# Performance work log

Measured on AMD Instinct MI355X. Metric: run time of the kernel, lower is better.

The kernel has to match this reference:

```python
import jax, jax.numpy as jnp
import numpy as np

N_NODES = 50000
N_EDGES = 800000
FEAT_DIM = 64
NUM_RELS = 8


def setup_inputs() -> dict:
    key = jax.random.key(0)
    k1, k2, k3, k4, k5 = jax.random.split(key, 5)
    features = jax.random.normal(k1, (N_NODES, FEAT_DIM), dtype=jnp.float32)
    # xavier_uniform with relu gain ~= sqrt(2)*sqrt(6/(D+D))
    limit = np.sqrt(2.0) * np.sqrt(6.0 / (FEAT_DIM + FEAT_DIM))
    weight_r = jax.random.uniform(k2, (NUM_RELS, FEAT_DIM, FEAT_DIM), dtype=jnp.float32,
                                  minval=-limit, maxval=limit)
    src = jax.random.randint(k3, (N_EDGES,), 0, N_NODES, dtype=jnp.int64 if jax.config.jax_enable_x64 else jnp.int32)
    dst = jax.random.randint(k4, (N_EDGES,), 0, N_NODES, dtype=src.dtype)
    etype = jax.random.randint(k5, (N_EDGES,), 0, NUM_RELS, dtype=src.dtype)
    return {"features": features, "weight_r": weight_r, "src": src, "dst": dst, "etype": etype}


def reference(features, weight_r, src, dst, etype):
    N, D = features.shape
    c = 0.2
    # in-degree of each destination node (DGL 'deg' node data)
    deg = jax.ops.segment_sum(jnp.ones(dst.shape, dtype=features.dtype), dst, num_segments=N)
    # relation-batched matmul: h @ W_r for every relation, then gather per edge.
    # [R, N, D] = 8*50000*64 floats -- cheap vs. materializing [E, D, D] weights.
    hw = jnp.einsum('nd,rdf->rnf', features, weight_r)
    msg = hw[etype, src] / deg[dst][:, None]          # [E, D]
    M = jax.ops.segment_sum(msg, dst, num_segments=N)  # scatter-sum mailbox reduce
    updated = jax.nn.relu(c * features + (1.0 - c) * M)
    # DGL only applies reduce to nodes that received messages; others keep h.
    return jnp.where((deg > 0)[:, None], updated, features)
```

## Files before the change

### kernel.cpp

```cpp
#include <hip/hip_runtime.h>
#include <hip/hip_bf16.h>

#define N_NODES 50000
#define N_EDGES 800000
#define FEAT 64
#define NRELS 8
#define NBUCK 196
#define EPB 2048
#define NBP 391
#define BCAP 5120
#define FB_BLOCKS 782
#define NPB 32
#define FUSE_BLOCKS 1563

typedef __attribute__((ext_vector_type(8))) short bf16x8;
typedef __attribute__((ext_vector_type(4))) float f32x4;

static __host__ __device__ inline size_t align256(size_t x) { return (x + 255) & ~(size_t)255; }

__device__ inline unsigned short f2b(float f) {
    unsigned u = __builtin_bit_cast(unsigned, f);
    unsigned r = (u + 0x7fffu + ((u >> 16) & 1u)) >> 16;
    return (unsigned short)r;
}
__device__ inline float b2f(unsigned short u) {
    unsigned v = ((unsigned)u) << 16;
    return __builtin_bit_cast(float, v);
}

__global__ void bfill_kernel(const int* __restrict__ dst, const int* __restrict__ srcv,
                             const int* __restrict__ et, const float* __restrict__ W,
                             int* __restrict__ bcnt, int* __restrict__ tmp,
                             unsigned short* __restrict__ WtT, int E) {
    __shared__ int hist[256];
    __shared__ int base[256];
    __shared__ int lcur[256];
    const int t = threadIdx.x;
    hist[t] = 0; lcur[t] = 0;
    __syncthreads();

    const int4* dst4 = (const int4*)dst;
    const int4* src4 = (const int4*)srcv;
    const int4* et4  = (const int4*)et;
    const int n4 = E >> 2;
    int bk[8], pk[8];
#pragma unroll
    for (int k = 0; k < 2; k++) {
        int i4 = blockIdx.x * 512 + t + k * 256;
        if (i4 < n4) {
            int4 d = dst4[i4];
            int4 s = src4[i4];
            int4 r = et4[i4];
            const int dd[4] = {d.x, d.y, d.z, d.w};
            const int ss[4] = {s.x, s.y, s.z, s.w};
            const int rr[4] = {r.x, r.y, r.z, r.w};
#pragma unroll
            for (int j = 0; j < 4; j++) {
                int idx = k * 4 + j;
                bk[idx] = dd[j] >> 8;
                pk[idx] = (ss[j] & 0xFFFF) | (rr[j] << 16) | ((dd[j] & 255) << 19);
                atomicAdd(&hist[bk[idx]], 1);
            }
        } else {
#pragma unroll
            for (int j = 0; j < 4; j++) bk[k * 4 + j] = -1;
        }
    }
    __syncthreads();
    if (t < NBUCK && hist[t] > 0)
        base[t] = t * BCAP + atomicAdd(&bcnt[t], hist[t]);
    __syncthreads();
#pragma unroll
    for (int k = 0; k < 8; k++) {
        if (bk[k] >= 0) {
            int r = atomicAdd(&lcur[bk[k]], 1);
            int pos = base[bk[k]] + r;
            if (pos < (bk[k] + 1) * BCAP)
                tmp[pos] = pk[k];
        }
    }

    if (blockIdx.x < 32) {
        int i4 = blockIdx.x * 256 + t;
        float4 v = ((const float4*)W)[i4];
        int bse = i4 * 4;
        int f0 = bse & 63;
        int rd = bse >> 6;
        int d  = rd & 63;
        int r  = rd >> 6;
        unsigned short* w0 = WtT + ((size_t)(r * 64 + f0) * 64 + d);
        w0[0 * 64] = f2b(v.x);
        w0[1 * 64] = f2b(v.y);
        w0[2 * 64] = f2b(v.z);
        w0[3 * 64] = f2b(v.w);
    }
}

__global__ void mid_kernel(const int* __restrict__ bcnt, const int* __restrict__ tmp,
                           int* __restrict__ spk, int* __restrict__ off_s,
                           int* __restrict__ off_e,
                           const float* __restrict__ feat,
                           unsigned short* __restrict__ Fb, int N) {
    __shared__ int hist[2048];
    __shared__ int s[256];
    const int t = threadIdx.x;

    if (blockIdx.x < NBUCK) {
        const int b = blockIdx.x;
        const int n0 = b * 256;
        const int nn = min(256, N - n0);
        const int s0 = b * BCAP;
        const int s1 = s0 + min(bcnt[b], BCAP);

#pragma unroll
        for (int j = 0; j < 8; j++) hist[t * 8 + j] = 0;
        __syncthreads();
        for (int i = s0 + t; i < s1; i += 1024) {
            int v0 = tmp[i];
            int v1 = (i + 256 < s1) ? tmp[i + 256] : -1;
            int v2 = (i + 512 < s1) ? tmp[i + 512] : -1;
            int v3 = (i + 768 < s1) ? tmp[i + 768] : -1;
            atomicAdd(&hist[(v0 >> 16) & 0x7FF], 1);
            if (v1 >= 0) atomicAdd(&hist[(v1 >> 16) & 0x7FF], 1);
            if (v2 >= 0) atomicAdd(&hist[(v2 >> 16) & 0x7FF], 1);
            if (v3 >= 0) atomicAdd(&hist[(v3 >> 16) & 0x7FF], 1);
        }
        __syncthreads();
        int loc[8], st[8], T = 0;
#pragma unroll
        for (int j = 0; j < 8; j++) loc[j] = hist[t * 8 + j];
#pragma unroll
        for (int j = 0; j < 8; j++) { st[j] = T; T += loc[j]; }
        s[t] = T;
        __syncthreads();
        for (int o = 1; o < 256; o <<= 1) {
            int u = (t >= o) ? s[t - o] : 0;
            __syncthreads();
            s[t] += u;
            __syncthreads();
        }
        const int base = s0 + s[t] - T;
        if (t < nn) {
            off_s[n0 + t] = base;
            off_e[n0 + t] = base + T;
        }
#pragma unroll
        for (int j = 0; j < 8; j++) hist[t * 8 + j] = base + st[j];
        __syncthreads();
        for (int i = s0 + t; i < s1; i += 1024) {
            int v0 = tmp[i];
            int v1 = (i + 256 < s1) ? tmp[i + 256] : -1;
            int v2 = (i + 512 < s1) ? tmp[i + 512] : -1;
            int v3 = (i + 768 < s1) ? tmp[i + 768] : -1;
            int p0 = atomicAdd(&hist[(v0 >> 16) & 0x7FF], 1);
            spk[p0] = v0;
            if (v1 >= 0) { int p1 = atomicAdd(&hist[(v1 >> 16) & 0x7FF], 1); spk[p1] = v1; }
            if (v2 >= 0) { int p2 = atomicAdd(&hist[(v2 >> 16) & 0x7FF], 1); spk[p2] = v2; }
            if (v3 >= 0) { int p3 = atomicAdd(&hist[(v3 >> 16) & 0x7FF], 1); spk[p3] = v3; }
        }
        return;
    }

    const int fbb = blockIdx.x - NBUCK;
    const int node = fbb * 64 + (t >> 2);
    if (node >= N) return;
    const int seg = t & 3;
    const float4* F4 = (const float4*)feat + (size_t)node * 16 + seg * 4;
    float4 v0 = F4[0], v1 = F4[1], v2 = F4[2], v3 = F4[3];
    bf16x8 b0, b1;
    b0[0] = (short)f2b(v0.x); b0[1] = (short)f2b(v0.y);
    b0[2] = (short)f2b(v0.z); b0[3] = (short)f2b(v0.w);
    b0[4] = (short)f2b(v1.x); b0[5] = (short)f2b(v1.y);
    b0[6] = (short)f2b(v1.z); b0[7] = (short)f2b(v1.w);
    b1[0] = (short)f2b(v2.x); b1[1] = (short)f2b(v2.y);
    b1[2] = (short)f2b(v2.z); b1[3] = (short)f2b(v2.w);
    b1[4] = (short)f2b(v3.x); b1[5] = (short)f2b(v3.y);
    b1[6] = (short)f2b(v3.z); b1[7] = (short)f2b(v3.w);
    *(bf16x8*)(Fb + (size_t)node * 64 + seg * 16)     = b0;
    *(bf16x8*)(Fb + (size_t)node * 64 + seg * 16 + 8) = b1;
}

__global__ __launch_bounds__(256, 4) void fuse_kernel(
    const int* __restrict__ off_s, const int* __restrict__ off_e,
    const int* __restrict__ spk, const unsigned short* __restrict__ Fb,
    const unsigned short* __restrict__ WtT, const float* __restrict__ feat,
    float* __restrict__ out, int N) {
    __shared__ unsigned short Sb[NRELS][NPB][64];
    const int t = threadIdx.x;
    const int n0 = blockIdx.x * NPB;
    const int nn = min(NPB, N - n0);

    {
        f32x4 z = {0.f, 0.f, 0.f, 0.f};
        f32x4* zp = (f32x4*)&Sb[0][0][0];
#pragma unroll
        for (int i = 0; i < 8; i++) zp[t + 256 * i] = z;
    }
    __syncthreads();

    const int gid = t >> 3, q = t & 7;
    if (gid < nn) {
        const int gn = n0 + gid;
        const int b = off_s[gn], e = off_e[gn];
        const int swz = (q ^ (gid & 7)) * 8;
        unsigned short* srow = &Sb[0][0][0] + (size_t)gid * 64 + swz;
        float a[8] = {0.f, 0.f, 0.f, 0.f, 0.f, 0.f, 0.f, 0.f};
        int curR = -1;

        auto flushS = [&](int rel) {
            bf16x8 v;
#pragma unroll
            for (int k = 0; k < 8; k++) v[k] = (short)f2b(a[k]);
            *(bf16x8*)(srow + (size_t)rel * (NPB * 64)) = v;
        };
        auto proc = [&](int pk, bf16x8 u) {
            if (pk < 0) return;
            int r_ = (pk >> 16) & 7;
            if (r_ != curR) {
                if (curR >= 0) flushS(curR);
                curR = r_;
#pragma unroll
                for (int k = 0; k < 8; k++) a[k] = b2f((unsigned short)u[k]);
            } else {
#pragma unroll
                for (int k = 0; k < 8; k++) a[k] += b2f((unsigned short)u[k]);
            }
        };
        auto ld = [&](int idx, int& pk, bf16x8& u) {
            if (idx < e) {
                pk = spk[idx];
                u = *(const bf16x8*)(Fb + (size_t)(pk & 0xFFFF) * 64 + q * 8);
            } else {
                pk = -1;
                u = (bf16x8){0, 0, 0, 0, 0, 0, 0, 0};
            }
        };

        int pk0, pk1, pk2, pk3;
        bf16x8 u0 = {0,0,0,0,0,0,0,0}, u1 = u0, u2 = u0, u3 = u0;
        ld(b, pk0, u0); ld(b + 1, pk1, u1); ld(b + 2, pk2, u2); ld(b + 3, pk3, u3);
        for (int i = b; i < e; i += 4) {
            int np0, np1, np2, np3;
            bf16x8 v0 = u0, v1 = u0, v2 = u0, v3 = u0;
            ld(i + 4, np0, v0); ld(i + 5, np1, v1);
            ld(i + 6, np2, v2); ld(i + 7, np3, v3);
            proc(pk0, u0); proc(pk1, u1); proc(pk2, u2); proc(pk3, u3);
            pk0 = np0; u0 = v0; pk1 = np1; u1 = v1;
            pk2 = np2; u2 = v2; pk3 = np3; u3 = v3;
        }
        if (curR >= 0) flushS(curR);
    }
    __syncthreads();

    const int w = t >> 6, l = t & 63, col = l & 15, quad = l >> 4;
    f32x4 acc0 = {0.f, 0.f, 0.f, 0.f}, acc1 = {0.f, 0.f, 0.f, 0.f};
    const int sw0 = (quad ^ (col & 7)) * 8;
    const int sw1 = ((quad + 4) ^ (col & 7)) * 8;
#pragma unroll
    for (int r = 0; r < NRELS; r++) {
        const unsigned short* wp = WtT + (size_t)r * 4096 + ((w * 16 + col) * 64 + quad * 8);
        bf16x8 b0 = *(const bf16x8*)wp;
        bf16x8 b1 = *(const bf16x8*)(wp + 32);
        const unsigned short* Sr = &Sb[0][0][0] + (size_t)r * (NPB * 64);
        bf16x8 a0 = *(const bf16x8*)&Sr[col * 64 + sw0];
        bf16x8 a1 = *(const bf16x8*)&Sr[col * 64 + sw1];
        bf16x8 c0 = *(const bf16x8*)&Sr[(16 + col) * 64 + sw0];
        bf16x8 c1 = *(const bf16x8*)&Sr[(16 + col) * 64 + sw1];
        acc0 = __builtin_amdgcn_mfma_f32_16x16x32_bf16(a0, b0, acc0, 0, 0, 0);
        acc0 = __builtin_amdgcn_mfma_f32_16x16x32_bf16(a1, b1, acc0, 0, 0, 0);
        acc1 = __builtin_amdgcn_mfma_f32_16x16x32_bf16(c0, b0, acc1, 0, 0, 0);
        acc1 = __builtin_amdgcn_mfma_f32_16x16x32_bf16(c1, b1, acc1, 0, 0, 0);
    }
    __syncthreads();

    float* C = (float*)&Sb[0][0][0];
#pragma unroll
    for (int i = 0; i < 4; i++) {
        C[(quad * 4 + i) * 72 + w * 16 + col]        = acc0[i];
        C[(16 + quad * 4 + i) * 72 + w * 16 + col]   = acc1[i];
    }
    __syncthreads();

    {
        const int n = t >> 3;
        if (n < nn) {
            const int gn = n0 + n;
            const int f0 = (t & 7) * 8;
            const int deg = off_e[gn] - off_s[gn];
            float4 m0 = *(const float4*)&C[n * 72 + f0];
            float4 m1 = *(const float4*)&C[n * 72 + f0 + 4];
            const float4* fp = (const float4*)feat + (size_t)gn * 16 + (f0 >> 2);
            float4 h0 = fp[0], h1 = fp[1];
            float4 r0, r1;
            if (deg > 0) {
                float inv = 0.8f / (float)deg;
                r0.x = fmaxf(0.2f * h0.x + m0.x * inv, 0.f);
                r0.y = fmaxf(0.2f * h0.y + m0.y * inv, 0.f);
                r0.z = fmaxf(0.2f * h0.z + m0.z * inv, 0.f);
                r0.w = fmaxf(0.2f * h0.w + m0.w * inv, 0.f);
                r1.x = fmaxf(0.2f * h1.x + m1.x * inv, 0.f);
                r1.y = fmaxf(0.2f * h1.y + m1.y * inv, 0.f);
                r1.z = fmaxf(0.2f * h1.z + m1.z * inv, 0.f);
                r1.w = fmaxf(0.2f * h1.w + m1.w * inv, 0.f);
            } else {
                r0 = h0; r1 = h1;
            }
            float4* op = (float4*)out + (size_t)gn * 16 + (f0 >> 2);
            op[0] = r0;
            op[1] = r1;
        }
    }
}

__global__ void degf_kernel(const int* __restrict__ dst, float* __restrict__ deg, int E) {
    int e = blockIdx.x * blockDim.x + threadIdx.x;
    if (e < E) atomicAdd(deg + dst[e], 1.0f);
}

__global__ void otf_kernel(const int* __restrict__ src, const int* __restrict__ dst,
                           const int* __restrict__ et, const float* __restrict__ feat,
                           const float* __restrict__ W, float* __restrict__ out, int E) {
    int wid = (blockIdx.x * blockDim.x + threadIdx.x) >> 6;
    int l = threadIdx.x & 63;
    if (wid >= E) return;
    int s = src[wid], dd = dst[wid], r = et[wid];
    float fv = feat[(size_t)s * 64 + l];
    const float* Wr = W + (size_t)r * 4096;
    float acc = 0.f;
#pragma unroll
    for (int d = 0; d < 64; d++) {
        float a = __shfl(fv, d);
        acc += a * Wr[d * 64 + l];
    }
    atomicAdd(out + (size_t)dd * 64 + l, acc);
}

__global__ void final_kernel(const float* __restrict__ feat, const float* __restrict__ deg,
                             float* __restrict__ out, int N) {
    int i = blockIdx.x * blockDim.x + threadIdx.x;
    if (i >= N * 16) return;
    int n = i >> 4;
    float d = deg[n];
    float4 f = ((const float4*)feat)[i];
    float4 m = ((float4*)out)[i];
    float4 res;
    if (d > 0.f) {
        float inv = 0.8f / d;
        res.x = fmaxf(0.2f * f.x + m.x * inv, 0.f);
        res.y = fmaxf(0.2f * f.y + m.y * inv, 0.f);
        res.z = fmaxf(0.2f * f.z + m.z * inv, 0.f);
        res.w = fmaxf(0.2f * f.w + m.w * inv, 0.f);
    } else {
        res = f;
    }
    ((float4*)out)[i] = res;
}

extern "C" void kernel_launch(void* const* d_in, const int* in_sizes, int n_in,
                              void* d_out, int out_size, void* d_ws, size_t ws_size,
                              hipStream_t stream) {
    const float* feat = (const float*)d_in[0];
    const float* W    = (const float*)d_in[1];
    const int*   src  = (const int*)d_in[2];
    const int*   dst  = (const int*)d_in[3];
    const int*   et   = (const int*)d_in[4];
    float* out = (float*)d_out;

    const int N = N_NODES, E = N_EDGES;

    char* p = (char*)d_ws;
    int* bcnt  = (int*)p;  p += align256((size_t)NBUCK * 4);
    int* off_s = (int*)p;  p += align256((size_t)N * 4);
    int* off_e = (int*)p;  p += align256((size_t)N * 4);
    int* tmp   = (int*)p;  p += align256((size_t)NBUCK * BCAP * 4);
    int* spk   = (int*)p;  p += align256((size_t)NBUCK * BCAP * 4);
    unsigned short* WtT = (unsigned short*)p;
    p += align256((size_t)NRELS * FEAT * FEAT * 2);
    unsigned short* Fb = (unsigned short*)p;
    p += align256((size_t)N * FEAT * 2);
    size_t need_full = (size_t)(p - (char*)d_ws);

    if (ws_size >= need_full) {
        hipMemsetAsync(bcnt, 0, (size_t)NBUCK * 4, stream);
        bfill_kernel<<<NBP, 256, 0, stream>>>(dst, src, et, W, bcnt, tmp, WtT, E);
        mid_kernel<<<NBUCK + FB_BLOCKS, 256, 0, stream>>>(bcnt, tmp, spk, off_s, off_e,
                                                          feat, Fb, N);
        fuse_kernel<<<FUSE_BLOCKS, 256, 0, stream>>>(off_s, off_e, spk, Fb, WtT,
                                                     feat, out, N);
    } else {
        float* deg = (float*)d_ws;
        hipMemsetAsync(out, 0, (size_t)N * FEAT * 4, stream);
        hipMemsetAsync(deg, 0, (size_t)N * 4, stream);
        degf_kernel<<<(E + 255) / 256, 256, 0, stream>>>(dst, deg, E);
        otf_kernel<<<(E + 3) / 4, 256, 0, stream>>>(src, dst, et, feat, W, out, E);
        final_kernel<<<(N * 16 + 255) / 256, 256, 0, stream>>>(feat, deg, out, N);
    }
}
```

Measured before the change: 142.1 us.

## Move bf16 feature conversion into bucket-fill kernel and batch edge-index loads via shuffles

The feature-to-bf16 conversion and weight transpose now run as extra blocks of the bucket-fill kernel instead of the counting-sort kernel, so the sort kernel launches only its 196 bucket blocks. Each bucket-fill block handles twice as many edges (4096) with half as many blocks. In the fused gather kernel, each 8-lane group loads the first 32 packed edge indices cooperatively and broadcasts them with shuffles, then runs an unrolled gather with 8-deep prefetch of feature rows, followed by a scalar tail loop. The aim is to reduce the serialized latency of the mid kernel and improve memory-level parallelism in the gather, at the cost of higher register pressure from the 32-entry index array and 8 prefetched vectors.

```diff
diff --git a/kernel.cpp b/kernel.cpp
--- a/kernel.cpp
+++ b/kernel.cpp
@@ -6,8 +6,8 @@
 #define FEAT 64
 #define NRELS 8
 #define NBUCK 196
-#define EPB 2048
-#define NBP 391
+#define EPB 4096
+#define NBP 196
 #define BCAP 5120
 #define FB_BLOCKS 782
 #define NPB 32
@@ -30,12 +30,50 @@
 
 __global__ void bfill_kernel(const int* __restrict__ dst, const int* __restrict__ srcv,
                              const int* __restrict__ et, const float* __restrict__ W,
+                             const float* __restrict__ feat,
                              int* __restrict__ bcnt, int* __restrict__ tmp,
-                             unsigned short* __restrict__ WtT, int E) {
+                             unsigned short* __restrict__ WtT,
+                             unsigned short* __restrict__ Fb, int E, int N) {
+    const int t = threadIdx.x;
+
+    if (blockIdx.x >= NBP) {
+        const int fbb = blockIdx.x - NBP;
+        if (fbb < 32) {
+            int i4 = fbb * 256 + t;
+            float4 v = ((const float4*)W)[i4];
+            int bse = i4 * 4;
+            int f0 = bse & 63;
+            int rd = bse >> 6;
+            int d  = rd & 63;
+            int r  = rd >> 6;
+            unsigned short* w0 = WtT + ((size_t)(r * 64 + f0) * 64 + d);
+            w0[0 * 64] = f2b(v.x);
+            w0[1 * 64] = f2b(v.y);
+            w0[2 * 64] = f2b(v.z);
+            w0[3 * 64] = f2b(v.w);
+        }
+        const int node = fbb * 64 + (t >> 2);
+        if (node >= N) return;
+        const int seg = t & 3;
+        const float4* F4 = (const float4*)feat + (size_t)node * 16 + seg * 4;
+        float4 v0 = F4[0], v1 = F4[1], v2 = F4[2], v3 = F4[3];
+        bf16x8 b0, b1;
+        b0[0] = (short)f2b(v0.x); b0[1] = (short)f2b(v0.y);
+        b0[2] = (short)f2b(v0.z); b0[3] = (short)f2b(v0.w);
+        b0[4] = (short)f2b(v1.x); b0[5] = (short)f2b(v1.y);
+        b0[6] = (short)f2b(v1.z); b0[7] = (short)f2b(v1.w);
+        b1[0] = (short)f2b(v2.x); b1[1] = (short)f2b(v2.y);
+        b1[2] = (short)f2b(v2.z); b1[3] = (short)f2b(v2.w);
+        b1[4] = (short)f2b(v3.x); b1[5] = (short)f2b(v3.y);
+        b1[6] = (short)f2b(v3.z); b1[7] = (short)f2b(v3.w);
+        *(bf16x8*)(Fb + (size_t)node * 64 + seg * 16)     = b0;
+        *(bf16x8*)(Fb + (size_t)node * 64 + seg * 16 + 8) = b1;
+        return;
+    }
+
     __shared__ int hist[256];
     __shared__ int base[256];
     __shared__ int lcur[256];
-    const int t = threadIdx.x;
     hist[t] = 0; lcur[t] = 0;
     __syncthreads();
 
@@ -43,10 +81,10 @@
     const int4* src4 = (const int4*)srcv;
     const int4* et4  = (const int4*)et;
     const int n4 = E >> 2;
-    int bk[8], pk[8];
-#pragma unroll
-    for (int k = 0; k < 2; k++) {
-        int i4 = blockIdx.x * 512 + t + k * 256;
+    int bk[16], pk[16];
+#pragma unroll
+    for (int k = 0; k < 4; k++) {
+        int i4 = blockIdx.x * 1024 + t + k * 256;
         if (i4 < n4) {
             int4 d = dst4[i4];
             int4 s = src4[i4];
@@ -71,7 +109,7 @@
         base[t] = t * BCAP + atomicAdd(&bcnt[t], hist[t]);
     __syncthreads();
 #pragma unroll
-    for (int k = 0; k < 8; k++) {
+    for (int k = 0; k < 16; k++) {
         if (bk[k] >= 0) {
             int r = atomicAdd(&lcur[bk[k]], 1);
             int pos = base[bk[k]] + r;
@@ -79,105 +117,67 @@
                 tmp[pos] = pk[k];
         }
     }
-
-    if (blockIdx.x < 32) {
-        int i4 = blockIdx.x * 256 + t;
-        float4 v = ((const float4*)W)[i4];
-        int bse = i4 * 4;
-        int f0 = bse & 63;
-        int rd = bse >> 6;
-        int d  = rd & 63;
-        int r  = rd >> 6;
-        unsigned short* w0 = WtT + ((size_t)(r * 64 + f0) * 64 + d);
-        w0[0 * 64] = f2b(v.x);
-        w0[1 * 64] = f2b(v.y);
-        w0[2 * 64] = f2b(v.z);
-        w0[3 * 64] = f2b(v.w);
-    }
 }
 
 __global__ void mid_kernel(const int* __restrict__ bcnt, const int* __restrict__ tmp,
                            int* __restrict__ spk, int* __restrict__ off_s,
-                           int* __restrict__ off_e,
-                           const float* __restrict__ feat,
-                           unsigned short* __restrict__ Fb, int N) {
+                           int* __restrict__ off_e, int N) {
     __shared__ int hist[2048];
     __shared__ int s[256];
     const int t = threadIdx.x;
 
-    if (blockIdx.x < NBUCK) {
-        const int b = blockIdx.x;
-        const int n0 = b * 256;
-        const int nn = min(256, N - n0);
-        const int s0 = b * BCAP;
-        const int s1 = s0 + min(bcnt[b], BCAP);
-
-#pragma unroll
-        for (int j = 0; j < 8; j++) hist[t * 8 + j] = 0;
+    const int b = blockIdx.x;
+    const int n0 = b * 256;
+    const int nn = min(256, N - n0);
+    const int s0 = b * BCAP;
+    const int s1 = s0 + min(bcnt[b], BCAP);
+
+#pragma unroll
+    for (int j = 0; j < 8; j++) hist[t * 8 + j] = 0;
+    __syncthreads();
+    for (int i = s0 + t; i < s1; i += 1024) {
+        int v0 = tmp[i];
+        int v1 = (i + 256 < s1) ? tmp[i + 256] : -1;
+        int v2 = (i + 512 < s1) ? tmp[i + 512] : -1;
+        int v3 = (i + 768 < s1) ? tmp[i + 768] : -1;
+        atomicAdd(&hist[(v0 >> 16) & 0x7FF], 1);
+        if (v1 >= 0) atomicAdd(&hist[(v1 >> 16) & 0x7FF], 1);
+        if (v2 >= 0) atomicAdd(&hist[(v2 >> 16) & 0x7FF], 1);
+        if (v3 >= 0) atomicAdd(&hist[(v3 >> 16) & 0x7FF], 1);
+    }
+    __syncthreads();
+    int loc[8], st[8], T = 0;
+#pragma unroll
+    for (int j = 0; j < 8; j++) loc[j] = hist[t * 8 + j];
+#pragma unroll
+    for (int j = 0; j < 8; j++) { st[j] = T; T += loc[j]; }
+    s[t] = T;
+    __syncthreads();
+    for (int o = 1; o < 256; o <<= 1) {
+        int u = (t >= o) ? s[t - o] : 0;
         __syncthreads();
-        for (int i = s0 + t; i < s1; i += 1024) {
-            int v0 = tmp[i];
-            int v1 = (i + 256 < s1) ? tmp[i + 256] : -1;
-            int v2 = (i + 512 < s1) ? tmp[i + 512] : -1;
-            int v3 = (i + 768 < s1) ? tmp[i + 768] : -1;
-            atomicAdd(&hist[(v0 >> 16) & 0x7FF], 1);
-            if (v1 >= 0) atomicAdd(&hist[(v1 >> 16) & 0x7FF], 1);
-            if (v2 >= 0) atomicAdd(&hist[(v2 >> 16) & 0x7FF], 1);
-            if (v3 >= 0) atomicAdd(&hist[(v3 >> 16) & 0x7FF], 1);
-        }
+        s[t] += u;
         __syncthreads();
-        int loc[8], st[8], T = 0;
-#pragma unroll
-        for (int j = 0; j < 8; j++) loc[j] = hist[t * 8 + j];
-#pragma unroll
-        for (int j = 0; j < 8; j++) { st[j] = T; T += loc[j]; }
-        s[t] = T;
-        __syncthreads();
-        for (int o = 1; o < 256; o <<= 1) {
-            int u = (t >= o) ? s[t - o] : 0;
-            __syncthreads();
-            s[t] += u;
-            __syncthreads();
-        }
-        const int base = s0 + s[t] - T;
-        if (t < nn) {
-            off_s[n0 + t] = base;
-            off_e[n0 + t] = base + T;
-        }
-#pragma unroll
-        for (int j = 0; j < 8; j++) hist[t * 8 + j] = base + st[j];
-        __syncthreads();
-        for (int i = s0 + t; i < s1; i += 1024) {
-            int v0 = tmp[i];
-            int v1 = (i + 256 < s1) ? tmp[i + 256] : -1;
-            int v2 = (i + 512 < s1) ? tmp[i + 512] : -1;
-            int v3 = (i + 768 < s1) ? tmp[i + 768] : -1;
-            int p0 = atomicAdd(&hist[(v0 >> 16) & 0x7FF], 1);
-            spk[p0] = v0;
-            if (v1 >= 0) { int p1 = atomicAdd(&hist[(v1 >> 16) & 0x7FF], 1); spk[p1] = v1; }
-            if (v2 >= 0) { int p2 = atomicAdd(&hist[(v2 >> 16) & 0x7FF], 1); spk[p2] = v2; }
-            if (v3 >= 0) { int p3 = atomicAdd(&hist[(v3 >> 16) & 0x7FF], 1); spk[p3] = v3; }
-        }
-        return;
-    }
-
-    const int fbb = blockIdx.x - NBUCK;
-    const int node = fbb * 64 + (t >> 2);
-    if (node >= N) return;
-    const int seg = t & 3;
-    const float4* F4 = (const float4*)feat + (size_t)node * 16 + seg * 4;
-    float4 v0 = F4[0], v1 = F4[1], v2 = F4[2], v3 = F4[3];
-    bf16x8 b0, b1;
-    b0[0] = (short)f2b(v0.x); b0[1] = (short)f2b(v0.y);
-    b0[2] = (short)f2b(v0.z); b0[3] = (short)f2b(v0.w);
-    b0[4] = (short)f2b(v1.x); b0[5] = (short)f2b(v1.y);
-    b0[6] = (short)f2b(v1.z); b0[7] = (short)f2b(v1.w);
-    b1[0] = (short)f2b(v2.x); b1[1] = (short)f2b(v2.y);
-    b1[2] = (short)f2b(v2.z); b1[3] = (short)f2b(v2.w);
-    b1[4] = (short)f2b(v3.x); b1[5] = (short)f2b(v3.y);
-    b1[6] = (short)f2b(v3.z); b1[7] = (short)f2b(v3.w);
-    *(bf16x8*)(Fb + (size_t)node * 64 + seg * 16)     = b0;
-    *(bf16x8*)(Fb + (size_t)node * 64 + seg * 16 + 8) = b1;
+    }
+    const int base = s0 + s[t] - T;
+    if (t < nn) {
+        off_s[n0 + t] = base;
+        off_e[n0 + t] = base + T;
+    }
+#pragma unroll
+    for (int j = 0; j < 8; j++) hist[t * 8 + j] = base + st[j];
+    __syncthreads();
+    for (int i = s0 + t; i < s1; i += 1024) {
+        int v0 = tmp[i];
+        int v1 = (i + 256 < s1) ? tmp[i + 256] : -1;
+        int v2 = (i + 512 < s1) ? tmp[i + 512] : -1;
+        int v3 = (i + 768 < s1) ? tmp[i + 768] : -1;
+        int p0 = atomicAdd(&hist[(v0 >> 16) & 0x7FF], 1);
+        spk[p0] = v0;
+        if (v1 >= 0) { int p1 = atomicAdd(&hist[(v1 >> 16) & 0x7FF], 1); spk[p1] = v1; }
+        if (v2 >= 0) { int p2 = atomicAdd(&hist[(v2 >> 16) & 0x7FF], 1); spk[p2] = v2; }
+        if (v3 >= 0) { int p3 = atomicAdd(&hist[(v3 >> 16) & 0x7FF], 1); spk[p3] = v3; }
+    }
 }
 
 __global__ __launch_bounds__(256, 4) void fuse_kernel(
@@ -199,6 +199,7 @@
     __syncthreads();
 
     const int gid = t >> 3, q = t & 7;
+    const int lanebase = (t & 63) & ~7;
     if (gid < nn) {
         const int gn = n0 + gid;
         const int b = off_s[gn], e = off_e[gn];
@@ -213,40 +214,60 @@
             for (int k = 0; k < 8; k++) v[k] = (short)f2b(a[k]);
             *(bf16x8*)(srow + (size_t)rel * (NPB * 64)) = v;
         };
-        auto proc = [&](int pk, bf16x8 u) {
-            if (pk < 0) return;
-            int r_ = (pk >> 16) & 7;
-            if (r_ != curR) {
+
+        int pks0 = (b + q      < e) ? spk[b + q]      : -1;
+        int pks1 = (b + q + 8  < e) ? spk[b + q + 8]  : -1;
+        int pks2 = (b + q + 16 < e) ? spk[b + q + 16] : -1;
+        int pks3 = (b + q + 24 < e) ? spk[b + q + 24] : -1;
+
+        int pkj[32];
+#pragma unroll
+        for (int j = 0; j < 8; j++) pkj[j]      = __shfl(pks0, lanebase | j);
+#pragma unroll
+        for (int j = 0; j < 8; j++) pkj[8 + j]  = __shfl(pks1, lanebase | j);
+#pragma unroll
+        for (int j = 0; j < 8; j++) pkj[16 + j] = __shfl(pks2, lanebase | j);
+#pragma unroll
+        for (int j = 0; j < 8; j++) pkj[24 + j] = __shfl(pks3, lanebase | j);
+
+        bf16x8 u[8];
+#pragma unroll
+        for (int j = 0; j < 8; j++) {
+            u[j] = (bf16x8){0, 0, 0, 0, 0, 0, 0, 0};
+            if (pkj[j] >= 0)
+                u[j] = *(const bf16x8*)(Fb + (size_t)(pkj[j] & 0xFFFF) * 64 + q * 8);
+        }
+#pragma unroll
+        for (int j = 0; j < 32; j++) {
+            bf16x8 uu = u[j & 7];
+            if (j + 8 < 32) {
+                if (pkj[j + 8] >= 0)
+                    u[j & 7] = *(const bf16x8*)(Fb + (size_t)(pkj[j + 8] & 0xFFFF) * 64 + q * 8);
+            }
+            if (pkj[j] >= 0) {
+                int rel = (pkj[j] >> 16) & 7;
+                if (rel != curR) {
+                    if (curR >= 0) flushS(curR);
+                    curR = rel;
+#pragma unroll
+                    for (int k = 0; k < 8; k++) a[k] = 0.f;
+                }
+#pragma unroll
+                for (int k = 0; k < 8; k++) a[k] += b2f((unsigned short)uu[k]);
+            }
+        }
+        for (int i = b + 32; i < e; i++) {
+            int pk = spk[i];
+            bf16x8 uu = *(const bf16x8*)(Fb + (size_t)(pk & 0xFFFF) * 64 + q * 8);
+            int rel = (pk >> 16) & 7;
+            if (rel != curR) {
                 if (curR >= 0) flushS(curR);
-                curR = r_;
-#pragma unroll
-                for (int k = 0; k < 8; k++) a[k] = b2f((unsigned short)u[k]);
-            } else {
-#pragma unroll
-                for (int k = 0; k < 8; k++) a[k] += b2f((unsigned short)u[k]);
+                curR = rel;
+#pragma unroll
+                for (int k = 0; k < 8; k++) a[k] = 0.f;
             }
-        };
-        auto ld = [&](int idx, int& pk, bf16x8& u) {
-            if (idx < e) {
-                pk = spk[idx];
-                u = *(const bf16x8*)(Fb + (size_t)(pk & 0xFFFF) * 64 + q * 8);
-            } else {
-                pk = -1;
-                u = (bf16x8){0, 0, 0, 0, 0, 0, 0, 0};
-            }
-        };
-
-        int pk0, pk1, pk2, pk3;
-        bf16x8 u0 = {0,0,0,0,0,0,0,0}, u1 = u0, u2 = u0, u3 = u0;
-        ld(b, pk0, u0); ld(b + 1, pk1, u1); ld(b + 2, pk2, u2); ld(b + 3, pk3, u3);
-        for (int i = b; i < e; i += 4) {
-            int np0, np1, np2, np3;
-            bf16x8 v0 = u0, v1 = u0, v2 = u0, v3 = u0;
-            ld(i + 4, np0, v0); ld(i + 5, np1, v1);
-            ld(i + 6, np2, v2); ld(i + 7, np3, v3);
-            proc(pk0, u0); proc(pk1, u1); proc(pk2, u2); proc(pk3, u3);
-            pk0 = np0; u0 = v0; pk1 = np1; u1 = v1;
-            pk2 = np2; u2 = v2; pk3 = np3; u3 = v3;
+#pragma unroll
+            for (int k = 0; k < 8; k++) a[k] += b2f((unsigned short)uu[k]);
         }
         if (curR >= 0) flushS(curR);
     }
@@ -382,9 +403,9 @@
 
     if (ws_size >= need_full) {
         hipMemsetAsync(bcnt, 0, (size_t)NBUCK * 4, stream);
-        bfill_kernel<<<NBP, 256, 0, stream>>>(dst, src, et, W, bcnt, tmp, WtT, E);
-        mid_kernel<<<NBUCK + FB_BLOCKS, 256, 0, stream>>>(bcnt, tmp, spk, off_s, off_e,
-                                                          feat, Fb, N);
+        bfill_kernel<<<NBP + FB_BLOCKS, 256, 0, stream>>>(dst, src, et, W, feat,
+                                                          bcnt, tmp, WtT, Fb, E, N);
+        mid_kernel<<<NBUCK, 256, 0, stream>>>(bcnt, tmp, spk, off_s, off_e, N);
         fuse_kernel<<<FUSE_BLOCKS, 256, 0, stream>>>(off_s, off_e, spk, Fb, WtT,
                                                      feat, out, N);
     } else {
```

Result: faster. 123.4 us (-13.2%).
